# Kernel optimization log

Hardware: AMD Instinct MI355X
Metric: run time of the kernel (lower is better)

The kernel has to match this reference:

```python
import jax, jax.numpy as jnp
import numpy as np

B, S, H, NH, HD = 2, 2048, 2048, 32, 64
ROPE_THETA = 10000.0


def _rope_tables(seq_len, head_dim, theta):
    inv_freq = 1.0 / (theta ** (jnp.arange(0, head_dim, 2, dtype=jnp.float32) / head_dim))
    t = jnp.arange(seq_len, dtype=jnp.float32)
    freqs = jnp.outer(t, inv_freq)                 # [S, HD/2]
    emb = jnp.concatenate([freqs, freqs], axis=-1)  # [S, HD]
    return jnp.cos(emb), jnp.sin(emb)


def setup_inputs() -> dict:
    key = jax.random.key(0)
    ks = jax.random.split(key, 6)
    cos, sin = _rope_tables(S, HD, ROPE_THETA)
    scale = 0.02
    return {
        "hidden_states": jax.random.normal(ks[0], (B, S, H), dtype=jnp.float32),
        "attention_mask": jnp.zeros((B, S), dtype=jnp.float32),
        "cos": cos,
        "sin": sin,
        "Wq": jax.random.normal(ks[1], (H, H), dtype=jnp.float32) * scale,
        "Wk": jax.random.normal(ks[2], (H, H), dtype=jnp.float32) * scale,
        "Wv": jax.random.normal(ks[3], (H, H), dtype=jnp.float32) * scale,
        "Wo": jax.random.normal(ks[4], (H, H), dtype=jnp.float32) * scale,
    }


def _rotate_half(x):
    x1, x2 = jnp.split(x, 2, axis=-1)
    return jnp.concatenate([-x2, x1], axis=-1)


def reference(hidden_states, attention_mask, cos, sin, Wq, Wk, Wv, Wo):
    b, s, _ = hidden_states.shape
    # QKV projections (nn.Linear: x @ W.T), reshape to [B, NH, S, HD]
    def proj(W):
        y = hidden_states @ W.T
        return y.reshape(b, s, NH, HD).transpose(0, 2, 1, 3)
    q, k, v = proj(Wq), proj(Wk), proj(Wv)
    # RoPE (HF rotate_half convention); cos/sin: [S, HD] -> broadcast [1,1,S,HD]
    c = cos[None, None, :, :]
    sn = sin[None, None, :, :]
    q = q * c + _rotate_half(q) * sn
    k = k * c + _rotate_half(k) * sn
    # attention: [B, NH, S, S]
    scores = jnp.einsum("bhqd,bhkd->bhqk", q, k) / jnp.sqrt(jnp.float32(HD))
    scores = scores + attention_mask[:, None, None, :]
    probs = jax.nn.softmax(scores, axis=-1)
    out = jnp.einsum("bhqk,bhkd->bhqd", probs, v)
    out = out.transpose(0, 2, 1, 3).reshape(b, s, NH * HD)
    return out @ Wo.T
```

## Files before the change

### kernel.cpp

```cpp
#include <hip/hip_runtime.h>
#include <stdint.h>
#include <math.h>

#define NB 2
#define SS 2048
#define HH 2048
#define NHH 32
#define HDD 64
#define MM (NB*SS)

typedef __attribute__((ext_vector_type(8))) short short8;
typedef __attribute__((ext_vector_type(4))) short short4v;
typedef __attribute__((ext_vector_type(4))) float f32x4;

#define GLOBAL_AS const __attribute__((address_space(1))) void*
#define LDS_AS __attribute__((address_space(3))) void*

static __device__ __forceinline__ short rne_bf16(float x) {
    uint32_t u = __builtin_bit_cast(uint32_t, x);
    u += 0x7FFFu + ((u >> 16) & 1u);
    return (short)(u >> 16);
}
static __device__ __forceinline__ float bf16f(short h) {
    return __builtin_bit_cast(float, (uint32_t)((uint16_t)h) << 16);
}
static __device__ __forceinline__ uint32_t pack_bf16_rne(float a, float b) {
    uint32_t ua = __builtin_bit_cast(uint32_t, a);
    uint32_t ub = __builtin_bit_cast(uint32_t, b);
    ua += 0x7FFFu + ((ua >> 16) & 1u);
    ub += 0x7FFFu + ((ub >> 16) & 1u);
    return __builtin_amdgcn_perm(ub, ua, 0x07060302);
}
static __device__ __forceinline__ uint32_t cvt_pk_bf16(float a, float b) {
    uint32_t r;
    asm("v_cvt_pk_bf16_f32 %0, %1, %2" : "=v"(r) : "v"(a), "v"(b));
    return r;
}
static __device__ __forceinline__ float fast_exp2(float x) {
    float r;
    asm("v_exp_f32 %0, %1" : "=v"(r) : "v"(x));
    return r;
}

__global__ void __launch_bounds__(256)
k_cvt(const float* __restrict__ in, short* __restrict__ out, int n4) {
    int i = blockIdx.x * blockDim.x + threadIdx.x;
    if (i >= n4) return;
    float4 f = reinterpret_cast<const float4*>(in)[i];
    short4v o;
    o.x = rne_bf16(f.x); o.y = rne_bf16(f.y);
    o.z = rne_bf16(f.z); o.w = rne_bf16(f.w);
    reinterpret_cast<short4v*>(out)[i] = o;
}

__global__ void __launch_bounds__(256)
k_cvt_split(const float* __restrict__ in, short* __restrict__ hi, short* __restrict__ lo, int n4) {
    int i = blockIdx.x * blockDim.x + threadIdx.x;
    if (i >= n4) return;
    float4 f = reinterpret_cast<const float4*>(in)[i];
    short4v h, l;
    h.x = rne_bf16(f.x); l.x = rne_bf16(f.x - bf16f(h.x));
    h.y = rne_bf16(f.y); l.y = rne_bf16(f.y - bf16f(h.y));
    h.z = rne_bf16(f.z); l.z = rne_bf16(f.z - bf16f(h.z));
    h.w = rne_bf16(f.w); l.w = rne_bf16(f.w - bf16f(h.w));
    reinterpret_cast<short4v*>(hi)[i] = h;
    reinterpret_cast<short4v*>(lo)[i] = l;
}

__global__ void __launch_bounds__(256, 2)
k_gemm_qkv(const short* __restrict__ X,
           const short* __restrict__ Wqh, const short* __restrict__ Wkh, const short* __restrict__ Wvh,
           const float* __restrict__ cosT, const float* __restrict__ sinT,
           short* __restrict__ Qr, short* __restrict__ Kr, short* __restrict__ Vt)
{
    __shared__ short lA[128 * 32];
    __shared__ short lBq[128 * 32];
    __shared__ short lBk[128 * 32];
    __shared__ short lBv[128 * 32];
    const int tid = threadIdx.x;
    const int lane = tid & 63;
    const int wave = tid >> 6;
    const int lrow = lane & 15;
    const int quad = lane >> 4;
    const int mblk = blockIdx.y * 128;
    const int nblk = blockIdx.x * 128;
    const int m0 = mblk + (wave >> 1) * 64;
    const int n0 = nblk + (wave & 1) * 64;
    const int mw = (wave >> 1) * 64;
    const int nw = (wave & 1) * 64;

    const int srow = wave * 32 + (lane >> 2);
    const int skc = (lane & 3) * 8;
    const short* gA = X   + (size_t)(mblk + srow) * HH + skc;
    const short* gQ = Wqh + (size_t)(nblk + srow) * HH + skc;
    const short* gK = Wkh + (size_t)(nblk + srow) * HH + skc;
    const short* gV = Wvh + (size_t)(nblk + srow) * HH + skc;
    const int lofs = wave * 1024;

    f32x4 acc[3][4][4];
    #pragma unroll
    for (int z = 0; z < 3; z++)
        #pragma unroll
        for (int i = 0; i < 4; i++)
            #pragma unroll
            for (int j = 0; j < 4; j++) acc[z][i][j] = 0.f;

    #pragma unroll 1
    for (int k0 = 0; k0 < HH; k0 += 32) {
        __syncthreads();
        #pragma unroll
        for (int j = 0; j < 2; j++) {
            size_t go = (size_t)j * 16 * HH + k0;
            int lo = lofs + j * 512;
            __builtin_amdgcn_global_load_lds((GLOBAL_AS)(gA + go), (LDS_AS)(&lA[lo]),  16, 0, 0);
            __builtin_amdgcn_global_load_lds((GLOBAL_AS)(gQ + go), (LDS_AS)(&lBq[lo]), 16, 0, 0);
            __builtin_amdgcn_global_load_lds((GLOBAL_AS)(gK + go), (LDS_AS)(&lBk[lo]), 16, 0, 0);
            __builtin_amdgcn_global_load_lds((GLOBAL_AS)(gV + go), (LDS_AS)(&lBv[lo]), 16, 0, 0);
        }
        __syncthreads();

        short8 a[4];
        #pragma unroll
        for (int mt = 0; mt < 4; mt++)
            a[mt] = *reinterpret_cast<const short8*>(&lA[(mw + mt * 16 + lrow) * 32 + quad * 8]);

        const short* lBz[3] = { lBq, lBk, lBv };
        #pragma unroll
        for (int z = 0; z < 3; z++) {
            short8 b[4];
            #pragma unroll
            for (int nt = 0; nt < 4; nt++)
                b[nt] = *reinterpret_cast<const short8*>(&lBz[z][(nw + nt * 16 + lrow) * 32 + quad * 8]);
            #pragma unroll
            for (int mt = 0; mt < 4; mt++)
                #pragma unroll
                for (int nt = 0; nt < 4; nt++)
                    acc[z][mt][nt] = __builtin_amdgcn_mfma_f32_16x16x32_bf16(a[mt], b[nt], acc[z][mt][nt], 0, 0, 0);
        }
    }

    const float QSCL = 0.18033688011112042f;

    #pragma unroll
    for (int z = 0; z < 3; z++) {
        #pragma unroll
        for (int mt = 0; mt < 4; mt++) {
            #pragma unroll
            for (int r = 0; r < 4; r++) {
                int row = m0 + mt * 16 + quad * 4 + r;
                int b_i = row >> 11;
                int s_i = row & (SS - 1);
                #pragma unroll
                for (int nt = 0; nt < 4; nt++) {
                    int col = n0 + nt * 16 + lrow;
                    int h_i = col >> 6;
                    int d_i = col & 63;
                    float v = acc[z][mt][nt][r];
                    if (z < 2) {
                        float pair = (nt & 2) ? acc[z][mt][nt - 2][r] : -acc[z][mt][nt + 2][r];
                        float c = cosT[s_i * HDD + d_i];
                        float sn = sinT[s_i * HDD + d_i];
                        v = v * c + pair * sn;
                        if (z == 0) v *= QSCL;
                        short* dst = (z == 0) ? Qr : Kr;
                        dst[(((size_t)b_i * NHH + h_i) * SS + s_i) * HDD + d_i] = rne_bf16(v);
                    } else {
                        Vt[(((size_t)b_i * NHH + h_i) * HDD + d_i) * SS + s_i] = rne_bf16(v);
                    }
                }
            }
        }
    }
}

__global__ void __launch_bounds__(256, 2)
k_attn(const short* __restrict__ Qr, const short* __restrict__ Kr, const short* __restrict__ Vt,
       const float* __restrict__ mask,
       short* __restrict__ Ah, short* __restrict__ Al)
{
    __shared__ short plds[4][4096];
    __shared__ short ldsK[2][4096];
    __shared__ short ldsV[2][4096];
    const int lane = threadIdx.x & 63;
    const int wave = threadIdx.x >> 6;
    const int lrow = lane & 15;
    const int quad = lane >> 4;
    const int aofs = lrow & 7;
    const int b = blockIdx.x >> 5;
    const int h = blockIdx.x & 31;
    const int q0w = blockIdx.y * 256 + wave * 64;

    const size_t bh = (size_t)b * NHH + h;
    const short* Qbase = Qr + bh * SS * HDD;
    const short* Kbase = Kr + bh * SS * HDD;
    const short* Vbase = Vt + bh * (size_t)HDD * SS;
    const float* mrow = mask + b * SS;
    char* cb = (char*)&plds[wave][0];

    const int strow = lane >> 3;
    const int stch  = (lane & 7) ^ strow;
    const short* Kst0 = Kbase + (size_t)(wave * 16 + strow)     * HDD + stch * 8;
    const short* Kst1 = Kbase + (size_t)(wave * 16 + 8 + strow) * HDD + stch * 8;
    const short* Vst0 = Vbase + (size_t)(wave * 16 + strow)     * SS  + stch * 8;
    const short* Vst1 = Vbase + (size_t)(wave * 16 + 8 + strow) * SS  + stch * 8;
    const int ldst0 = wave * 1024;
    const int ldst1 = wave * 1024 + 512;

#define STAGE_KV(buf, kk) do { \
    __builtin_amdgcn_global_load_lds((GLOBAL_AS)(Kst0 + (size_t)(kk) * HDD), (LDS_AS)(&ldsK[buf][ldst0]), 16, 0, 0); \
    __builtin_amdgcn_global_load_lds((GLOBAL_AS)(Kst1 + (size_t)(kk) * HDD), (LDS_AS)(&ldsK[buf][ldst1]), 16, 0, 0); \
    __builtin_amdgcn_global_load_lds((GLOBAL_AS)(Vst0 + (kk)), (LDS_AS)(&ldsV[buf][ldst0]), 16, 0, 0); \
    __builtin_amdgcn_global_load_lds((GLOBAL_AS)(Vst1 + (kk)), (LDS_AS)(&ldsV[buf][ldst1]), 16, 0, 0); \
} while (0)

    short8 qf[4][2];
    #pragma unroll
    for (int nt = 0; nt < 4; nt++)
        #pragma unroll
        for (int c = 0; c < 2; c++)
            qf[nt][c] = *reinterpret_cast<const short8*>(
                Qbase + (size_t)(q0w + nt * 16 + lrow) * HDD + c * 32 + quad * 8);

    short8 onesf;
    #pragma unroll
    for (int i = 0; i < 8; i++) onesf[i] = (short)0x3F80;

    f32x4 oacc[4][4];
    f32x4 lacc[4];
    #pragma unroll
    for (int i = 0; i < 4; i++) {
        lacc[i] = 0.f;
        #pragma unroll
        for (int j = 0; j < 4; j++) oacc[i][j] = 0.f;
    }

    const float L2E = 1.44269504f;

    STAGE_KV(0, 0);
    asm volatile("s_waitcnt vmcnt(0)" ::: "memory");
    __syncthreads();

    int cur = 0;
    #pragma unroll 1
    for (int k0 = 0; k0 < SS; k0 += 64) {
        if (k0 + 64 < SS) STAGE_KV(cur ^ 1, k0 + 64);

        short8 kf[4][2];
        #pragma unroll
        for (int kt = 0; kt < 4; kt++)
            #pragma unroll
            for (int c = 0; c < 2; c++)
                kf[kt][c] = *reinterpret_cast<const short8*>(
                    &ldsK[cur][(kt * 16 + lrow) * 64 + (((4 * c + quad) ^ aofs) * 8)]);

        f32x4 sacc[4][4];
        #pragma unroll
        for (int kt = 0; kt < 4; kt++)
            #pragma unroll
            for (int nt = 0; nt < 4; nt++) {
                f32x4 z4 = 0.f;
                z4 = __builtin_amdgcn_mfma_f32_16x16x32_bf16(kf[kt][0], qf[nt][0], z4, 0, 0, 0);
                sacc[kt][nt] = __builtin_amdgcn_mfma_f32_16x16x32_bf16(kf[kt][1], qf[nt][1], z4, 0, 0, 0);
            }

        asm volatile("s_waitcnt lgkmcnt(0)" ::: "memory");

        #pragma unroll
        for (int kt = 0; kt < 4; kt++) {
            float4 mk = *reinterpret_cast<const float4*>(mrow + k0 + kt * 16 + quad * 4);
            float m0v = mk.x * L2E, m1v = mk.y * L2E, m2v = mk.z * L2E, m3v = mk.w * L2E;
            #pragma unroll
            for (int nt = 0; nt < 4; nt++) {
                float p0 = fast_exp2(sacc[kt][nt][0] + m0v);
                float p1 = fast_exp2(sacc[kt][nt][1] + m1v);
                float p2 = fast_exp2(sacc[kt][nt][2] + m2v);
                float p3 = fast_exp2(sacc[kt][nt][3] + m3v);
                uint2 w;
                w.x = cvt_pk_bf16(p0, p1);
                w.y = cvt_pk_bf16(p2, p3);
                *reinterpret_cast<uint2*>(
                    cb + (nt * 16 + lrow) * 128 +
                    (((2 * kt + (quad >> 1)) ^ aofs) * 16) + (quad & 1) * 8) = w;
            }
        }

        asm volatile("s_waitcnt lgkmcnt(0)" ::: "memory");

        #pragma unroll
        for (int c = 0; c < 2; c++) {
            short8 pf[4], vf[4];
            #pragma unroll
            for (int mt = 0; mt < 4; mt++)
                pf[mt] = *reinterpret_cast<const short8*>(
                    cb + (mt * 16 + lrow) * 128 + (((4 * c + quad) ^ aofs) * 16));
            #pragma unroll
            for (int dt = 0; dt < 4; dt++)
                vf[dt] = *reinterpret_cast<const short8*>(
                    &ldsV[cur][(dt * 16 + lrow) * 64 + (((4 * c + quad) ^ aofs) * 8)]);
            #pragma unroll
            for (int mt = 0; mt < 4; mt++) {
                lacc[mt] = __builtin_amdgcn_mfma_f32_16x16x32_bf16(pf[mt], onesf, lacc[mt], 0, 0, 0);
                #pragma unroll
                for (int dt = 0; dt < 4; dt++)
                    oacc[mt][dt] = __builtin_amdgcn_mfma_f32_16x16x32_bf16(pf[mt], vf[dt], oacc[mt][dt], 0, 0, 0);
            }
        }

        asm volatile("s_waitcnt vmcnt(0)" ::: "memory");
        __syncthreads();
        cur ^= 1;
    }
#undef STAGE_KV

    float linv[4][4];
    #pragma unroll
    for (int mt = 0; mt < 4; mt++)
        #pragma unroll
        for (int r = 0; r < 4; r++)
            linv[mt][r] = 1.f / lacc[mt][r];

    #pragma unroll
    for (int mt = 0; mt < 4; mt++) {
        #pragma unroll
        for (int r = 0; r < 4; r++) {
            int s_i = q0w + mt * 16 + quad * 4 + r;
            size_t row = (size_t)b * SS + s_i;
            #pragma unroll
            for (int dt = 0; dt < 4; dt++) {
                float x = oacc[mt][dt][r] * linv[mt][r];
                short hi = rne_bf16(x);
                short lo = rne_bf16(x - bf16f(hi));
                size_t idx = row * HH + (size_t)h * 64 + dt * 16 + lrow;
                Ah[idx] = hi;
                Al[idx] = lo;
            }
        }
    }
}

__global__ void __launch_bounds__(256, 2)
k_gemm_wo(const short* __restrict__ Ahh, const short* __restrict__ All,
          const short* __restrict__ Bhh, const short* __restrict__ Bll,
          float* __restrict__ C)
{
    __shared__ short lAh[128 * 32];
    __shared__ short lAl[128 * 32];
    __shared__ short lBh[128 * 32];
    __shared__ short lBl[128 * 32];
    const int tid = threadIdx.x;
    const int lane = tid & 63;
    const int wave = tid >> 6;
    const int lrow = lane & 15;
    const int quad = lane >> 4;
    const int mblk = blockIdx.y * 128;
    const int nblk = blockIdx.x * 128;
    const int m0 = mblk + (wave >> 1) * 64;
    const int n0 = nblk + (wave & 1) * 64;
    const int mw = (wave >> 1) * 64;
    const int nw = (wave & 1) * 64;

    const int srow = wave * 32 + (lane >> 2);
    const int skc = (lane & 3) * 8;
    const short* gAh = Ahh + (size_t)(mblk + srow) * HH + skc;
    const short* gAl = All + (size_t)(mblk + srow) * HH + skc;
    const short* gBh = Bhh + (size_t)(nblk + srow) * HH + skc;
    const short* gBl = Bll + (size_t)(nblk + srow) * HH + skc;
    short* lAhw = &lAh[wave * 1024];
    short* lAlw = &lAl[wave * 1024];
    short* lBhw = &lBh[wave * 1024];
    short* lBlw = &lBl[wave * 1024];

    f32x4 acc[4][4];
    #pragma unroll
    for (int i = 0; i < 4; i++)
        #pragma unroll
        for (int j = 0; j < 4; j++) acc[i][j] = 0.f;

    #pragma unroll 1
    for (int k0 = 0; k0 < HH; k0 += 32) {
        __syncthreads();
        #pragma unroll
        for (int j = 0; j < 2; j++) {
            size_t go = (size_t)j * 16 * HH + k0;
            __builtin_amdgcn_global_load_lds((GLOBAL_AS)(gAh + go), (LDS_AS)(lAhw + j * 512), 16, 0, 0);
            __builtin_amdgcn_global_load_lds((GLOBAL_AS)(gAl + go), (LDS_AS)(lAlw + j * 512), 16, 0, 0);
            __builtin_amdgcn_global_load_lds((GLOBAL_AS)(gBh + go), (LDS_AS)(lBhw + j * 512), 16, 0, 0);
            __builtin_amdgcn_global_load_lds((GLOBAL_AS)(gBl + go), (LDS_AS)(lBlw + j * 512), 16, 0, 0);
        }
        __syncthreads();

        short8 ah[4], al[4], bh[4], bl[4];
        #pragma unroll
        for (int mt = 0; mt < 4; mt++) {
            int off = (mw + mt * 16 + lrow) * 32 + quad * 8;
            ah[mt] = *reinterpret_cast<const short8*>(&lAh[off]);
            al[mt] = *reinterpret_cast<const short8*>(&lAl[off]);
        }
        #pragma unroll
        for (int nt = 0; nt < 4; nt++) {
            int off = (nw + nt * 16 + lrow) * 32 + quad * 8;
            bh[nt] = *reinterpret_cast<const short8*>(&lBh[off]);
            bl[nt] = *reinterpret_cast<const short8*>(&lBl[off]);
        }
        #pragma unroll
        for (int mt = 0; mt < 4; mt++)
            #pragma unroll
            for (int nt = 0; nt < 4; nt++) {
                acc[mt][nt] = __builtin_amdgcn_mfma_f32_16x16x32_bf16(ah[mt], bh[nt], acc[mt][nt], 0, 0, 0);
                acc[mt][nt] = __builtin_amdgcn_mfma_f32_16x16x32_bf16(al[mt], bh[nt], acc[mt][nt], 0, 0, 0);
                acc[mt][nt] = __builtin_amdgcn_mfma_f32_16x16x32_bf16(ah[mt], bl[nt], acc[mt][nt], 0, 0, 0);
            }
    }

    #pragma unroll
    for (int mt = 0; mt < 4; mt++)
        #pragma unroll
        for (int r = 0; r < 4; r++) {
            int row = m0 + mt * 16 + quad * 4 + r;
            #pragma unroll
            for (int nt = 0; nt < 4; nt++) {
                int col = n0 + nt * 16 + lrow;
                C[(size_t)row * HH + col] = acc[mt][nt][r];
            }
        }
}

extern "C" void kernel_launch(void* const* d_in, const int* in_sizes, int n_in,
                              void* d_out, int out_size, void* d_ws, size_t ws_size,
                              hipStream_t stream) {
    const float* hidden = (const float*)d_in[0];
    const float* maskp  = (const float*)d_in[1];
    const float* cosT   = (const float*)d_in[2];
    const float* sinT   = (const float*)d_in[3];
    const float* Wq     = (const float*)d_in[4];
    const float* Wk     = (const float*)d_in[5];
    const float* Wv     = (const float*)d_in[6];
    const float* Wo     = (const float*)d_in[7];
    float* out = (float*)d_out;

    char* ws = (char*)d_ws;
    auto alloc = [&](size_t bytes) {
        char* p = ws;
        ws += (bytes + 255) & ~(size_t)255;
        return p;
    };
    const size_t XB = (size_t)MM * HH * sizeof(short);
    const size_t WB = (size_t)HH * HH * sizeof(short);
    short* Xh  = (short*)alloc(XB);
    short* Wqh = (short*)alloc(WB);
    short* Wkh = (short*)alloc(WB);
    short* Wvh = (short*)alloc(WB);
    short* Woh = (short*)alloc(WB);
    short* Wol = (short*)alloc(WB);
    short* Qr  = (short*)alloc(XB);
    short* Kr  = (short*)alloc(XB);
    short* Vt  = (short*)alloc(XB);
    short* Ah  = (short*)alloc(XB);
    short* Al  = (short*)alloc(XB);

    const int nX4 = MM * HH / 4;
    const int nW4 = HH * HH / 4;
    k_cvt<<<dim3(nX4 / 256), dim3(256), 0, stream>>>(hidden, Xh, nX4);
    k_cvt<<<dim3(nW4 / 256), dim3(256), 0, stream>>>(Wq, Wqh, nW4);
    k_cvt<<<dim3(nW4 / 256), dim3(256), 0, stream>>>(Wk, Wkh, nW4);
    k_cvt<<<dim3(nW4 / 256), dim3(256), 0, stream>>>(Wv, Wvh, nW4);
    k_cvt_split<<<dim3(nW4 / 256), dim3(256), 0, stream>>>(Wo, Woh, Wol, nW4);

    k_gemm_qkv<<<dim3(HH / 128, MM / 128), dim3(256), 0, stream>>>(
        Xh, Wqh, Wkh, Wvh, cosT, sinT, Qr, Kr, Vt);

    k_attn<<<dim3(NB * NHH, SS / 256), dim3(256), 0, stream>>>(
        Qr, Kr, Vt, maskp, Ah, Al);

    k_gemm_wo<<<dim3(HH / 128, MM / 128), dim3(256), 0, stream>>>(
        Ah, Al, Woh, Wol, out);
}
```

Baseline: 437.0 us.

## Fuse conversion kernels, double GEMM K-tile with XOR-swizzled LDS and grouped block order

The five fp32-to-bf16 conversion launches are merged into one kernel that picks its source by index range. Both projection GEMMs now stage a K=64 slice per iteration instead of K=32, halving the number of barrier-separated load rounds. LDS columns are XOR-swizzled to avoid bank conflicts on the wider rows, and block indices are remapped so neighbouring blocks share weight tiles for better L2 reuse. The cost is doubled LDS per block (64KB in the QKV GEMM), which may limit how many blocks fit per CU.

Measured after the change: 402.3 us (median of 4 runs). 1.09x faster.

```diff
diff --git a/kernel.cpp b/kernel.cpp
--- a/kernel.cpp
+++ b/kernel.cpp
@@ -24,13 +24,6 @@
 static __device__ __forceinline__ float bf16f(short h) {
     return __builtin_bit_cast(float, (uint32_t)((uint16_t)h) << 16);
 }
-static __device__ __forceinline__ uint32_t pack_bf16_rne(float a, float b) {
-    uint32_t ua = __builtin_bit_cast(uint32_t, a);
-    uint32_t ub = __builtin_bit_cast(uint32_t, b);
-    ua += 0x7FFFu + ((ua >> 16) & 1u);
-    ub += 0x7FFFu + ((ub >> 16) & 1u);
-    return __builtin_amdgcn_perm(ub, ua, 0x07060302);
-}
 static __device__ __forceinline__ uint32_t cvt_pk_bf16(float a, float b) {
     uint32_t r;
     asm("v_cvt_pk_bf16_f32 %0, %1, %2" : "=v"(r) : "v"(a), "v"(b));
@@ -42,29 +35,40 @@
     return r;
 }
 
+#define N4X  2097152
+#define N4W  1048576
 __global__ void __launch_bounds__(256)
-k_cvt(const float* __restrict__ in, short* __restrict__ out, int n4) {
+k_cvt_all(const float* __restrict__ X, const float* __restrict__ Wq,
+          const float* __restrict__ Wk, const float* __restrict__ Wv,
+          const float* __restrict__ Wo,
+          short* __restrict__ Xh, short* __restrict__ Wqh, short* __restrict__ Wkh,
+          short* __restrict__ Wvh, short* __restrict__ Woh, short* __restrict__ Wol)
+{
     int i = blockIdx.x * blockDim.x + threadIdx.x;
-    if (i >= n4) return;
-    float4 f = reinterpret_cast<const float4*>(in)[i];
+    const float* src;
+    short* dst;
+    int j = i;
+    if (i < N4X)                { src = X;  dst = Xh;  }
+    else if (i < N4X + N4W)     { src = Wq; dst = Wqh; j = i - N4X; }
+    else if (i < N4X + 2*N4W)   { src = Wk; dst = Wkh; j = i - N4X - N4W; }
+    else if (i < N4X + 3*N4W)   { src = Wv; dst = Wvh; j = i - N4X - 2*N4W; }
+    else {
+        j = i - N4X - 3*N4W;
+        float4 f = reinterpret_cast<const float4*>(Wo)[j];
+        short4v h, l;
+        h.x = rne_bf16(f.x); l.x = rne_bf16(f.x - bf16f(h.x));
+        h.y = rne_bf16(f.y); l.y = rne_bf16(f.y - bf16f(h.y));
+        h.z = rne_bf16(f.z); l.z = rne_bf16(f.z - bf16f(h.z));
+        h.w = rne_bf16(f.w); l.w = rne_bf16(f.w - bf16f(h.w));
+        reinterpret_cast<short4v*>(Woh)[j] = h;
+        reinterpret_cast<short4v*>(Wol)[j] = l;
+        return;
+    }
+    float4 f = reinterpret_cast<const float4*>(src)[j];
     short4v o;
     o.x = rne_bf16(f.x); o.y = rne_bf16(f.y);
     o.z = rne_bf16(f.z); o.w = rne_bf16(f.w);
-    reinterpret_cast<short4v*>(out)[i] = o;
-}
-
-__global__ void __launch_bounds__(256)
-k_cvt_split(const float* __restrict__ in, short* __restrict__ hi, short* __restrict__ lo, int n4) {
-    int i = blockIdx.x * blockDim.x + threadIdx.x;
-    if (i >= n4) return;
-    float4 f = reinterpret_cast<const float4*>(in)[i];
-    short4v h, l;
-    h.x = rne_bf16(f.x); l.x = rne_bf16(f.x - bf16f(h.x));
-    h.y = rne_bf16(f.y); l.y = rne_bf16(f.y - bf16f(h.y));
-    h.z = rne_bf16(f.z); l.z = rne_bf16(f.z - bf16f(h.z));
-    h.w = rne_bf16(f.w); l.w = rne_bf16(f.w - bf16f(h.w));
-    reinterpret_cast<short4v*>(hi)[i] = h;
-    reinterpret_cast<short4v*>(lo)[i] = l;
+    reinterpret_cast<short4v*>(dst)[j] = o;
 }
 
 __global__ void __launch_bounds__(256, 2)
@@ -73,29 +77,33 @@
            const float* __restrict__ cosT, const float* __restrict__ sinT,
            short* __restrict__ Qr, short* __restrict__ Kr, short* __restrict__ Vt)
 {
-    __shared__ short lA[128 * 32];
-    __shared__ short lBq[128 * 32];
-    __shared__ short lBk[128 * 32];
-    __shared__ short lBv[128 * 32];
+    __shared__ short lA[128 * 64];
+    __shared__ short lBq[128 * 64];
+    __shared__ short lBk[128 * 64];
+    __shared__ short lBv[128 * 64];
     const int tid = threadIdx.x;
     const int lane = tid & 63;
     const int wave = tid >> 6;
     const int lrow = lane & 15;
     const int quad = lane >> 4;
-    const int mblk = blockIdx.y * 128;
-    const int nblk = blockIdx.x * 128;
+    const int swz = lrow & 7;
+
+    const int lin = blockIdx.y * 16 + blockIdx.x;
+    const int pos = lin >> 3;
+    const int nblk = ((lin & 7) * 2 + (pos & 1)) * 128;
+    const int mblk = (pos >> 1) * 128;
     const int m0 = mblk + (wave >> 1) * 64;
     const int n0 = nblk + (wave & 1) * 64;
     const int mw = (wave >> 1) * 64;
     const int nw = (wave & 1) * 64;
 
-    const int srow = wave * 32 + (lane >> 2);
-    const int skc = (lane & 3) * 8;
+    const int srow = wave * 32 + (lane >> 3);
+    const int skc = ((lane & 7) ^ (lane >> 3)) * 8;
     const short* gA = X   + (size_t)(mblk + srow) * HH + skc;
     const short* gQ = Wqh + (size_t)(nblk + srow) * HH + skc;
     const short* gK = Wkh + (size_t)(nblk + srow) * HH + skc;
     const short* gV = Wvh + (size_t)(nblk + srow) * HH + skc;
-    const int lofs = wave * 1024;
+    const int lofs = wave * 2048;
 
     f32x4 acc[3][4][4];
     #pragma unroll
@@ -106,11 +114,11 @@
             for (int j = 0; j < 4; j++) acc[z][i][j] = 0.f;
 
     #pragma unroll 1
-    for (int k0 = 0; k0 < HH; k0 += 32) {
+    for (int k0 = 0; k0 < HH; k0 += 64) {
         __syncthreads();
         #pragma unroll
-        for (int j = 0; j < 2; j++) {
-            size_t go = (size_t)j * 16 * HH + k0;
+        for (int j = 0; j < 4; j++) {
+            size_t go = (size_t)j * 8 * HH + k0;
             int lo = lofs + j * 512;
             __builtin_amdgcn_global_load_lds((GLOBAL_AS)(gA + go), (LDS_AS)(&lA[lo]),  16, 0, 0);
             __builtin_amdgcn_global_load_lds((GLOBAL_AS)(gQ + go), (LDS_AS)(&lBq[lo]), 16, 0, 0);
@@ -119,23 +127,26 @@
         }
         __syncthreads();
 
-        short8 a[4];
-        #pragma unroll
-        for (int mt = 0; mt < 4; mt++)
-            a[mt] = *reinterpret_cast<const short8*>(&lA[(mw + mt * 16 + lrow) * 32 + quad * 8]);
-
         const short* lBz[3] = { lBq, lBk, lBv };
         #pragma unroll
-        for (int z = 0; z < 3; z++) {
-            short8 b[4];
-            #pragma unroll
-            for (int nt = 0; nt < 4; nt++)
-                b[nt] = *reinterpret_cast<const short8*>(&lBz[z][(nw + nt * 16 + lrow) * 32 + quad * 8]);
+        for (int kk = 0; kk < 2; kk++) {
+            const int csl = ((kk * 4 + quad) ^ swz) * 8;
+            short8 a[4];
             #pragma unroll
             for (int mt = 0; mt < 4; mt++)
+                a[mt] = *reinterpret_cast<const short8*>(&lA[(mw + mt * 16 + lrow) * 64 + csl]);
+            #pragma unroll
+            for (int z = 0; z < 3; z++) {
+                short8 b[4];
                 #pragma unroll
                 for (int nt = 0; nt < 4; nt++)
-                    acc[z][mt][nt] = __builtin_amdgcn_mfma_f32_16x16x32_bf16(a[mt], b[nt], acc[z][mt][nt], 0, 0, 0);
+                    b[nt] = *reinterpret_cast<const short8*>(&lBz[z][(nw + nt * 16 + lrow) * 64 + csl]);
+                #pragma unroll
+                for (int mt = 0; mt < 4; mt++)
+                    #pragma unroll
+                    for (int nt = 0; nt < 4; nt++)
+                        acc[z][mt][nt] = __builtin_amdgcn_mfma_f32_16x16x32_bf16(a[mt], b[nt], acc[z][mt][nt], 0, 0, 0);
+            }
         }
     }
 
@@ -343,32 +354,36 @@
           const short* __restrict__ Bhh, const short* __restrict__ Bll,
           float* __restrict__ C)
 {
-    __shared__ short lAh[128 * 32];
-    __shared__ short lAl[128 * 32];
-    __shared__ short lBh[128 * 32];
-    __shared__ short lBl[128 * 32];
+    __shared__ short lAh[128 * 64];
+    __shared__ short lAl[128 * 64];
+    __shared__ short lBh[128 * 64];
+    __shared__ short lBl[128 * 64];
     const int tid = threadIdx.x;
     const int lane = tid & 63;
     const int wave = tid >> 6;
     const int lrow = lane & 15;
     const int quad = lane >> 4;
-    const int mblk = blockIdx.y * 128;
-    const int nblk = blockIdx.x * 128;
+    const int swz = lrow & 7;
+
+    const int lin = blockIdx.y * 16 + blockIdx.x;
+    const int pos = lin >> 3;
+    const int nblk = ((lin & 7) * 2 + (pos & 1)) * 128;
+    const int mblk = (pos >> 1) * 128;
     const int m0 = mblk + (wave >> 1) * 64;
     const int n0 = nblk + (wave & 1) * 64;
     const int mw = (wave >> 1) * 64;
     const int nw = (wave & 1) * 64;
 
-    const int srow = wave * 32 + (lane >> 2);
-    const int skc = (lane & 3) * 8;
+    const int srow = wave * 32 + (lane >> 3);
+    const int skc = ((lane & 7) ^ (lane >> 3)) * 8;
     const short* gAh = Ahh + (size_t)(mblk + srow) * HH + skc;
     const short* gAl = All + (size_t)(mblk + srow) * HH + skc;
     const short* gBh = Bhh + (size_t)(nblk + srow) * HH + skc;
     const short* gBl = Bll + (size_t)(nblk + srow) * HH + skc;
-    short* lAhw = &lAh[wave * 1024];
-    short* lAlw = &lAl[wave * 1024];
-    short* lBhw = &lBh[wave * 1024];
-    short* lBlw = &lBl[wave * 1024];
+    short* lAhw = &lAh[wave * 2048];
+    short* lAlw = &lAl[wave * 2048];
+    short* lBhw = &lBh[wave * 2048];
+    short* lBlw = &lBl[wave * 2048];
 
     f32x4 acc[4][4];
     #pragma unroll
@@ -377,11 +392,11 @@
         for (int j = 0; j < 4; j++) acc[i][j] = 0.f;
 
     #pragma unroll 1
-    for (int k0 = 0; k0 < HH; k0 += 32) {
+    for (int k0 = 0; k0 < HH; k0 += 64) {
         __syncthreads();
         #pragma unroll
-        for (int j = 0; j < 2; j++) {
-            size_t go = (size_t)j * 16 * HH + k0;
+        for (int j = 0; j < 4; j++) {
+            size_t go = (size_t)j * 8 * HH + k0;
             __builtin_amdgcn_global_load_lds((GLOBAL_AS)(gAh + go), (LDS_AS)(lAhw + j * 512), 16, 0, 0);
             __builtin_amdgcn_global_load_lds((GLOBAL_AS)(gAl + go), (LDS_AS)(lAlw + j * 512), 16, 0, 0);
             __builtin_amdgcn_global_load_lds((GLOBAL_AS)(gBh + go), (LDS_AS)(lBhw + j * 512), 16, 0, 0);
@@ -389,27 +404,31 @@
         }
         __syncthreads();
 
-        short8 ah[4], al[4], bh[4], bl[4];
-        #pragma unroll
-        for (int mt = 0; mt < 4; mt++) {
-            int off = (mw + mt * 16 + lrow) * 32 + quad * 8;
-            ah[mt] = *reinterpret_cast<const short8*>(&lAh[off]);
-            al[mt] = *reinterpret_cast<const short8*>(&lAl[off]);
-        }
-        #pragma unroll
-        for (int nt = 0; nt < 4; nt++) {
-            int off = (nw + nt * 16 + lrow) * 32 + quad * 8;
-            bh[nt] = *reinterpret_cast<const short8*>(&lBh[off]);
-            bl[nt] = *reinterpret_cast<const short8*>(&lBl[off]);
-        }
-        #pragma unroll
-        for (int mt = 0; mt < 4; mt++)
+        #pragma unroll
+        for (int kk = 0; kk < 2; kk++) {
+            const int csl = ((kk * 4 + quad) ^ swz) * 8;
+            short8 ah[4], al[4], bh[4], bl[4];
+            #pragma unroll
+            for (int mt = 0; mt < 4; mt++) {
+                int off = (mw + mt * 16 + lrow) * 64 + csl;
+                ah[mt] = *reinterpret_cast<const short8*>(&lAh[off]);
+                al[mt] = *reinterpret_cast<const short8*>(&lAl[off]);
+            }
             #pragma unroll
             for (int nt = 0; nt < 4; nt++) {
-                acc[mt][nt] = __builtin_amdgcn_mfma_f32_16x16x32_bf16(ah[mt], bh[nt], acc[mt][nt], 0, 0, 0);
-                acc[mt][nt] = __builtin_amdgcn_mfma_f32_16x16x32_bf16(al[mt], bh[nt], acc[mt][nt], 0, 0, 0);
-                acc[mt][nt] = __builtin_amdgcn_mfma_f32_16x16x32_bf16(ah[mt], bl[nt], acc[mt][nt], 0, 0, 0);
-            }
+                int off = (nw + nt * 16 + lrow) * 64 + csl;
+                bh[nt] = *reinterpret_cast<const short8*>(&lBh[off]);
+                bl[nt] = *reinterpret_cast<const short8*>(&lBl[off]);
+            }
+            #pragma unroll
+            for (int mt = 0; mt < 4; mt++)
+                #pragma unroll
+                for (int nt = 0; nt < 4; nt++) {
+                    acc[mt][nt] = __builtin_amdgcn_mfma_f32_16x16x32_bf16(ah[mt], bh[nt], acc[mt][nt], 0, 0, 0);
+                    acc[mt][nt] = __builtin_amdgcn_mfma_f32_16x16x32_bf16(al[mt], bh[nt], acc[mt][nt], 0, 0, 0);
+                    acc[mt][nt] = __builtin_amdgcn_mfma_f32_16x16x32_bf16(ah[mt], bl[nt], acc[mt][nt], 0, 0, 0);
+                }
+        }
     }
 
     #pragma unroll
@@ -458,13 +477,9 @@
     short* Ah  = (short*)alloc(XB);
     short* Al  = (short*)alloc(XB);
 
-    const int nX4 = MM * HH / 4;
-    const int nW4 = HH * HH / 4;
-    k_cvt<<<dim3(nX4 / 256), dim3(256), 0, stream>>>(hidden, Xh, nX4);
-    k_cvt<<<dim3(nW4 / 256), dim3(256), 0, stream>>>(Wq, Wqh, nW4);
-    k_cvt<<<dim3(nW4 / 256), dim3(256), 0, stream>>>(Wk, Wkh, nW4);
-    k_cvt<<<dim3(nW4 / 256), dim3(256), 0, stream>>>(Wv, Wvh, nW4);
-    k_cvt_split<<<dim3(nW4 / 256), dim3(256), 0, stream>>>(Wo, Woh, Wol, nW4);
+    const int nAll = N4X + 4 * N4W;
+    k_cvt_all<<<dim3(nAll / 256), dim3(256), 0, stream>>>(
+        hidden, Wq, Wk, Wv, Wo, Xh, Wqh, Wkh, Wvh, Woh, Wol);
 
     k_gemm_qkv<<<dim3(HH / 128, MM / 128), dim3(256), 0, stream>>>(
         Xh, Wqh, Wkh, Wvh, cosT, sinT, Qr, Kr, Vt);
```
